# Kernel optimization log

Measured on AMD Instinct MI355X. Metric: run time of the kernel, lower is better.

Reference implementation:

```python
import jax, jax.numpy as jnp
import numpy as np

N_NODES = 50000
N_EDGES = 800000
IN_FEATS = 128
HIDDEN = 128
DNN_H = 256
N_CLASSES = 40


def setup_inputs() -> dict:
    key = jax.random.key(0)
    ks = jax.random.split(key, 12)
    features = jax.random.normal(ks[0], (N_NODES, IN_FEATS), dtype=jnp.float32)
    src = jax.random.randint(ks[1], (N_EDGES,), 0, N_NODES, dtype=jnp.int32)
    dst = jax.random.randint(ks[2], (N_EDGES,), 0, N_NODES, dtype=jnp.int32)
    def lin(k, fi, fo):
        s = 1.0 / np.sqrt(fi)
        return jax.random.uniform(k, (fi, fo), jnp.float32, -s, s)
    W1 = lin(ks[3], IN_FEATS, HIDDEN)
    b1 = jnp.zeros((HIDDEN,), jnp.float32)
    W2 = lin(ks[4], HIDDEN, HIDDEN)
    b2 = jnp.zeros((HIDDEN,), jnp.float32)
    Wd1 = lin(ks[5], HIDDEN, DNN_H)
    bd1 = jnp.zeros((DNN_H,), jnp.float32)
    Wd2 = lin(ks[6], DNN_H, N_CLASSES)
    bd2 = jnp.zeros((N_CLASSES,), jnp.float32)
    return {"features": features, "src": src, "dst": dst,
            "W1": W1, "b1": b1, "W2": W2, "b2": b2,
            "Wd1": Wd1, "bd1": bd1, "Wd2": Wd2, "bd2": bd2}


def _graph_conv(x, src, dst, W, b):
    # dgl GraphConv, norm='both': D_out^{-1/2} -> sum-aggregate -> D_in^{-1/2} -> linear -> relu
    ones = jnp.ones((src.shape[0],), x.dtype)
    deg_out = jax.ops.segment_sum(ones, src, num_segments=N_NODES)
    deg_in = jax.ops.segment_sum(ones, dst, num_segments=N_NODES)
    inv_sqrt_out = jax.lax.rsqrt(jnp.maximum(deg_out, 1.0))  # clamp zero-degree to 1 like dgl
    inv_sqrt_in = jax.lax.rsqrt(jnp.maximum(deg_in, 1.0))
    x = x * inv_sqrt_out[:, None]
    h = jax.ops.segment_sum(x[src], dst, num_segments=N_NODES)  # [N, d] sparse SpMM
    h = h * inv_sqrt_in[:, None]
    return jax.nn.relu(h @ W + b)


def reference(features, src, dst, W1, b1, W2, b2, Wd1, bd1, Wd2, bd2):
    h = _graph_conv(features, src, dst, W1, b1)   # dropout = identity (eval)
    h = _graph_conv(h, src, dst, W2, b2)
    # DNN: Linear -> LeakyReLU(0.01) -> (dropout identity), x2
    h = jax.nn.leaky_relu(h @ Wd1 + bd1, negative_slope=0.01)
    h = jax.nn.leaky_relu(h @ Wd2 + bd2, negative_slope=0.01)
    return h
```

## Files before the change

kernel.cpp:

```cpp
#include <hip/hip_runtime.h>


#define SCAN_B 256

typedef __attribute__((ext_vector_type(8))) short short8v;
typedef __attribute__((ext_vector_type(4))) float f32x4;

__global__ void k_scanA(const int* __restrict__ deg_in, int* __restrict__ incl,
                        int* __restrict__ bsum, int N) {
    __shared__ int s[SCAN_B];
    int t = threadIdx.x, i = blockIdx.x * SCAN_B + t;
    int v = (i < N) ? deg_in[i] : 0;
    s[t] = v; __syncthreads();
    for (int o = 1; o < SCAN_B; o <<= 1) {
        int x = (t >= o) ? s[t - o] : 0;
        __syncthreads();
        s[t] += x;
        __syncthreads();
    }
    if (i < N) incl[i] = s[t];
    if (t == SCAN_B - 1) bsum[blockIdx.x] = s[t];
}

__global__ void k_scanB(int* __restrict__ bsum, int NB) {
    __shared__ int s[SCAN_B];
    int t = threadIdx.x;
    int v = (t < NB) ? bsum[t] : 0;
    s[t] = v; __syncthreads();
    for (int o = 1; o < SCAN_B; o <<= 1) {
        int x = (t >= o) ? s[t - o] : 0;
        __syncthreads();
        s[t] += x;
        __syncthreads();
    }
    if (t < NB) bsum[t] = s[t] - v;
}

__global__ void k_scanC(const int* __restrict__ deg_in, const int* __restrict__ deg_out,
                        int* __restrict__ row_ptr, const int* __restrict__ bsum,
                        float* __restrict__ inv_in, float* __restrict__ inv_out,
                        int N, int E) {
    int t = threadIdx.x, i = blockIdx.x * SCAN_B + t;
    if (i < N) {
        int di = deg_in[i];
        row_ptr[i] = row_ptr[i] - di + bsum[blockIdx.x];
        inv_in[i]  = rsqrtf(fmaxf((float)di, 1.0f));
        inv_out[i] = rsqrtf(fmaxf((float)deg_out[i], 1.0f));
    }
    if (i == 0) row_ptr[N] = E;
}

__global__ void k_scatter3(const int* __restrict__ src, const int* __restrict__ dst,
                           const int* __restrict__ row_ptr, const int* __restrict__ rank,
                           const float* __restrict__ inv_out,
                           int2* __restrict__ edges, int E) {
    int i = blockIdx.x * blockDim.x + threadIdx.x;
    if (i < E) {
        int s = src[i];
        int2 p;
        p.x = s;
        p.y = __float_as_int(inv_out[s]);
        edges[row_ptr[dst[i]] + rank[i]] = p;
    }
}

__global__ void k_gather2(const float* __restrict__ X, const int2* __restrict__ edges,
                          const int* __restrict__ row_ptr, const float* __restrict__ inv_in,
                          const float* __restrict__ bias, float* __restrict__ Y, int N) {
    int lane = threadIdx.x & 31;
    int row = blockIdx.x * 8 + (threadIdx.x >> 5);
    if (row >= N) return;
    int rs = row_ptr[row], re = row_ptr[row + 1];
    float4 acc = {0.f, 0.f, 0.f, 0.f};
    int e = rs;
    #define LDROW(s) (*reinterpret_cast<const float4*>(&X[(size_t)(s) * 128 + lane * 4]))
    for (; e + 8 <= re; e += 8) {
        int2 p0 = edges[e],     p1 = edges[e + 1], p2 = edges[e + 2], p3 = edges[e + 3];
        int2 p4 = edges[e + 4], p5 = edges[e + 5], p6 = edges[e + 6], p7 = edges[e + 7];
        float4 x0 = LDROW(p0.x), x1 = LDROW(p1.x), x2 = LDROW(p2.x), x3 = LDROW(p3.x);
        float4 x4 = LDROW(p4.x), x5 = LDROW(p5.x), x6 = LDROW(p6.x), x7 = LDROW(p7.x);
        float c0 = __int_as_float(p0.y), c1 = __int_as_float(p1.y);
        float c2 = __int_as_float(p2.y), c3 = __int_as_float(p3.y);
        float c4 = __int_as_float(p4.y), c5 = __int_as_float(p5.y);
        float c6 = __int_as_float(p6.y), c7 = __int_as_float(p7.y);
        acc.x += c0*x0.x + c1*x1.x + c2*x2.x + c3*x3.x + c4*x4.x + c5*x5.x + c6*x6.x + c7*x7.x;
        acc.y += c0*x0.y + c1*x1.y + c2*x2.y + c3*x3.y + c4*x4.y + c5*x5.y + c6*x6.y + c7*x7.y;
        acc.z += c0*x0.z + c1*x1.z + c2*x2.z + c3*x3.z + c4*x4.z + c5*x5.z + c6*x6.z + c7*x7.z;
        acc.w += c0*x0.w + c1*x1.w + c2*x2.w + c3*x3.w + c4*x4.w + c5*x5.w + c6*x6.w + c7*x7.w;
    }
    for (; e + 4 <= re; e += 4) {
        int2 p0 = edges[e], p1 = edges[e + 1], p2 = edges[e + 2], p3 = edges[e + 3];
        float4 x0 = LDROW(p0.x), x1 = LDROW(p1.x), x2 = LDROW(p2.x), x3 = LDROW(p3.x);
        float c0 = __int_as_float(p0.y), c1 = __int_as_float(p1.y);
        float c2 = __int_as_float(p2.y), c3 = __int_as_float(p3.y);
        acc.x += c0*x0.x + c1*x1.x + c2*x2.x + c3*x3.x;
        acc.y += c0*x0.y + c1*x1.y + c2*x2.y + c3*x3.y;
        acc.z += c0*x0.z + c1*x1.z + c2*x2.z + c3*x3.z;
        acc.w += c0*x0.w + c1*x1.w + c2*x2.w + c3*x3.w;
    }
    for (; e < re; ++e) {
        int2 p = edges[e];
        float c = __int_as_float(p.y);
        float4 xv = LDROW(p.x);
        acc.x += c * xv.x; acc.y += c * xv.y; acc.z += c * xv.z; acc.w += c * xv.w;
    }
    #undef LDROW
    float si = inv_in[row];
    float4 b4 = *reinterpret_cast<const float4*>(&bias[lane * 4]);
    float4 o;
    o.x = fmaxf(fmaf(acc.x, si, b4.x), 0.f);
    o.y = fmaxf(fmaf(acc.y, si, b4.y), 0.f);
    o.z = fmaxf(fmaf(acc.z, si, b4.z), 0.f);
    o.w = fmaxf(fmaf(acc.w, si, b4.w), 0.f);
    *reinterpret_cast<float4*>(&Y[(size_t)row * 128 + lane * 4]) = o;
}

__device__ inline unsigned short bf16_rne(float f) {
    unsigned int u = __float_as_uint(f);
    u += 0x7fffu + ((u >> 16) & 1u);
    return (unsigned short)(u >> 16);
}

__device__ inline void split1(float a, unsigned short& h, unsigned short& l) {
    unsigned short hh = bf16_rne(a);
    float hf = __uint_as_float((unsigned int)hh << 16);
    l = bf16_rne(a - hf);
    h = hh;
}

template<int K, int N, int ACT, bool DEG>
__global__ __launch_bounds__(256) void k_gemm_mfma(const float* __restrict__ A,
                                                   const float* __restrict__ W,
                                                   const float* __restrict__ bias,
                                                   float* __restrict__ C, int M,
                                                   const int* __restrict__ src,
                                                   const int* __restrict__ dst,
                                                   int* __restrict__ deg_out,
                                                   int* __restrict__ deg_in,
                                                   int* __restrict__ rank, int E, int epb,
                                                   int gmm, int degb) {
    __shared__ unsigned short Bh[64 * K], Bl[64 * K];
    __shared__ unsigned short Ah[128 * 32], Al[128 * 32];

    int t = threadIdx.x;
    int m0, cb;
    if (DEG) {
        int bid = blockIdx.x;
        if (bid < degb) {
            int base = bid * epb;
            int end = min(E, base + epb);
            for (int i = base + t; i < end; i += 256) {
                atomicAdd(&deg_out[src[i]], 1);
                rank[i] = atomicAdd(&deg_in[dst[i]], 1);
            }
            return;
        }
        int tile = bid - degb;
        m0 = (tile % gmm) * 128;
        cb = (tile / gmm) * 64;
    } else {
        m0 = blockIdx.x * 128;
        cb = blockIdx.y * 64;
    }

    {
        int c = t & 63;
        int kb = (t >> 6) * (K / 4);
        bool cok = (N % 64 == 0) || (cb + c < N);
        for (int j = 0; j < K / 4; ++j) {
            int k = kb + j;
            float v = cok ? W[(size_t)k * N + cb + c] : 0.f;
            unsigned short hi, lo; split1(v, hi, lo);
            int byte = (c * 2 * K + 2 * k) ^ ((c & 7) << 4);
            Bh[byte >> 1] = hi;
            Bl[byte >> 1] = lo;
        }
    }

    f32x4 acc[4][2];
    #pragma unroll
    for (int i = 0; i < 4; ++i)
        #pragma unroll
        for (int j = 0; j < 2; ++j)
            acc[i][j] = (f32x4){0.f, 0.f, 0.f, 0.f};

    int lane = t & 63;
    int wave = t >> 6;
    int wm = wave >> 1, wn = wave & 1;
    int lr = lane & 15, lg = lane >> 4;

    for (int kt = 0; kt < K / 32; ++kt) {
        __syncthreads();
        #pragma unroll
        for (int i = 0; i < 4; ++i) {
            int g = i * 256 + t;
            int r = g >> 3;
            int kq = (g & 7) * 4;
            int gr = m0 + r;
            float4 v = {0.f, 0.f, 0.f, 0.f};
            if (gr < M) v = *reinterpret_cast<const float4*>(&A[(size_t)gr * K + kt * 32 + kq]);
            ushort4 h4, l4;
            split1(v.x, h4.x, l4.x);
            split1(v.y, h4.y, l4.y);
            split1(v.z, h4.z, l4.z);
            split1(v.w, h4.w, l4.w);
            int byte = (r * 64 + 2 * kq) ^ ((r & 7) << 4);
            *reinterpret_cast<ushort4*>(&Ah[byte >> 1]) = h4;
            *reinterpret_cast<ushort4*>(&Al[byte >> 1]) = l4;
        }
        __syncthreads();

        short8v bhf[2], blf[2];
        #pragma unroll
        for (int nf = 0; nf < 2; ++nf) {
            int c = wn * 32 + nf * 16 + lr;
            int byte = (c * 2 * K + 2 * (kt * 32 + lg * 8)) ^ ((c & 7) << 4);
            bhf[nf] = *reinterpret_cast<const short8v*>(&Bh[byte >> 1]);
            blf[nf] = *reinterpret_cast<const short8v*>(&Bl[byte >> 1]);
        }
        #pragma unroll
        for (int mf = 0; mf < 4; ++mf) {
            int r = wm * 64 + mf * 16 + lr;
            int byte = (r * 64 + 2 * (lg * 8)) ^ ((r & 7) << 4);
            short8v ahf = *reinterpret_cast<const short8v*>(&Ah[byte >> 1]);
            short8v alf = *reinterpret_cast<const short8v*>(&Al[byte >> 1]);
            #pragma unroll
            for (int nf = 0; nf < 2; ++nf) {
                acc[mf][nf] = __builtin_amdgcn_mfma_f32_16x16x32_bf16(ahf, bhf[nf], acc[mf][nf], 0, 0, 0);
                acc[mf][nf] = __builtin_amdgcn_mfma_f32_16x16x32_bf16(ahf, blf[nf], acc[mf][nf], 0, 0, 0);
                acc[mf][nf] = __builtin_amdgcn_mfma_f32_16x16x32_bf16(alf, bhf[nf], acc[mf][nf], 0, 0, 0);
            }
        }
    }

    #pragma unroll
    for (int mf = 0; mf < 4; ++mf) {
        #pragma unroll
        for (int nf = 0; nf < 2; ++nf) {
            int col = cb + wn * 32 + nf * 16 + lr;
            if ((N % 64 != 0) && col >= N) continue;
            float bv = (ACT < 2) ? bias[col] : 0.f;
            #pragma unroll
            for (int rg = 0; rg < 4; ++rg) {
                int row = m0 + wm * 64 + mf * 16 + lg * 4 + rg;
                if (row < M) {
                    float v = acc[mf][nf][rg];
                    if (ACT == 0) v = fmaxf(v + bv, 0.f);
                    else if (ACT == 1) { v += bv; v = (v > 0.f) ? v : 0.01f * v; }
                    C[(size_t)row * N + col] = v;
                }
            }
        }
    }
}

extern "C" void kernel_launch(void* const* d_in, const int* in_sizes, int n_in,
                              void* d_out, int out_size, void* d_ws, size_t ws_size,
                              hipStream_t stream) {
    const float* feat = (const float*)d_in[0];
    const int*   src  = (const int*)d_in[1];
    const int*   dst  = (const int*)d_in[2];
    const float* W1   = (const float*)d_in[3];
    const float* b1   = (const float*)d_in[4];
    const float* W2   = (const float*)d_in[5];
    const float* b2   = (const float*)d_in[6];
    const float* Wd1  = (const float*)d_in[7];
    const float* bd1  = (const float*)d_in[8];
    const float* Wd2  = (const float*)d_in[9];
    const float* bd2  = (const float*)d_in[10];
    float* out = (float*)d_out;

    const int N = in_sizes[0] / 128;
    const int E = in_sizes[1];

    char* ws = (char*)d_ws;
    size_t off = 0;
    auto alloc = [&](size_t bytes) -> void* {
        void* p = ws + off;
        off += (bytes + 255) & ~(size_t)255;
        return p;
    };
    int* deg_out  = (int*)alloc((size_t)N * 4);
    int* deg_in   = (int*)alloc((size_t)N * 4);
    int* row_ptr  = (int*)alloc((size_t)(N + 1) * 4);
    int* bsum     = (int*)alloc(SCAN_B * 4);
    int* rank     = (int*)alloc((size_t)E * 4);
    int2* edges   = (int2*)alloc((size_t)E * 8);
    float* inv_out = (float*)alloc((size_t)N * 4);
    float* inv_in  = (float*)alloc((size_t)N * 4);
    float* bufA = (float*)alloc((size_t)N * 128 * 4);
    float* bufB = (float*)alloc((size_t)N * 128 * 4);
    float* hd   = (float*)alloc((size_t)N * 256 * 4);

    size_t zspan = (char*)deg_in + (size_t)N * 4 - (char*)deg_out;
    hipMemsetAsync(deg_out, 0, zspan, stream);

    int gE = (E + 255) / 256;
    int gN = (N + SCAN_B - 1) / SCAN_B;
    int gG = (N + 7) / 8;
    int gMM = (N + 127) / 128;

    const int DEGB = 512;
    int epb = (E + DEGB - 1) / DEGB;
    k_gemm_mfma<128, 128, 2, true><<<DEGB + gMM * 2, 256, 0, stream>>>(
        feat, W1, nullptr, bufA, N, src, dst, deg_out, deg_in, rank, E, epb, gMM, DEGB);

    k_scanA<<<gN, SCAN_B, 0, stream>>>(deg_in, row_ptr, bsum, N);
    k_scanB<<<1, SCAN_B, 0, stream>>>(bsum, gN);
    k_scanC<<<gN, SCAN_B, 0, stream>>>(deg_in, deg_out, row_ptr, bsum, inv_in, inv_out, N, E);
    k_scatter3<<<gE, 256, 0, stream>>>(src, dst, row_ptr, rank, inv_out, edges, E);

    k_gather2<<<gG, 256, 0, stream>>>(bufA, edges, row_ptr, inv_in, b1, bufB, N);
    k_gemm_mfma<128, 128, 2, false><<<dim3(gMM, 2), 256, 0, stream>>>(
        bufB, W2, nullptr, bufA, N, nullptr, nullptr, nullptr, nullptr, nullptr, 0, 0, 0, 0);
    k_gather2<<<gG, 256, 0, stream>>>(bufA, edges, row_ptr, inv_in, b2, bufB, N);
    k_gemm_mfma<128, 256, 1, false><<<dim3(gMM, 4), 256, 0, stream>>>(
        bufB, Wd1, bd1, hd, N, nullptr, nullptr, nullptr, nullptr, nullptr, 0, 0, 0, 0);
    k_gemm_mfma<256, 40, 1, false><<<dim3(gMM, 1), 256, 0, stream>>>(
        hd, Wd2, bd2, out, N, nullptr, nullptr, nullptr, nullptr, nullptr, 0, 0, 0, 0);
}
```

Baseline: 337.3 us.

## Fuse SpMM gather with following dense GEMM into one gconv kernel

Replaces each gather-then-GEMM pair with a single kernel. It aggregates 64 rows of neighbour features, applies bias and ReLU, splits the result to bf16 hi/lo in shared memory, and multiplies by the next weight matrix with MFMA. This drops the intermediate round trip of the N×128 activation through global memory and one launch per layer. In exchange the gather phase runs with fewer blocks (64 rows per block) and each block reloads the weights, which may cut latency hiding during the irregular gather. The degree-counting loop is also unrolled by four so more loads and atomics are in flight.

Result: slower. 470.2 us (+39.4%).

```diff
diff --git a/kernel.cpp b/kernel.cpp
--- a/kernel.cpp
+++ b/kernel.cpp
@@ -64,57 +64,6 @@
     }
 }
 
-__global__ void k_gather2(const float* __restrict__ X, const int2* __restrict__ edges,
-                          const int* __restrict__ row_ptr, const float* __restrict__ inv_in,
-                          const float* __restrict__ bias, float* __restrict__ Y, int N) {
-    int lane = threadIdx.x & 31;
-    int row = blockIdx.x * 8 + (threadIdx.x >> 5);
-    if (row >= N) return;
-    int rs = row_ptr[row], re = row_ptr[row + 1];
-    float4 acc = {0.f, 0.f, 0.f, 0.f};
-    int e = rs;
-    #define LDROW(s) (*reinterpret_cast<const float4*>(&X[(size_t)(s) * 128 + lane * 4]))
-    for (; e + 8 <= re; e += 8) {
-        int2 p0 = edges[e],     p1 = edges[e + 1], p2 = edges[e + 2], p3 = edges[e + 3];
-        int2 p4 = edges[e + 4], p5 = edges[e + 5], p6 = edges[e + 6], p7 = edges[e + 7];
-        float4 x0 = LDROW(p0.x), x1 = LDROW(p1.x), x2 = LDROW(p2.x), x3 = LDROW(p3.x);
-        float4 x4 = LDROW(p4.x), x5 = LDROW(p5.x), x6 = LDROW(p6.x), x7 = LDROW(p7.x);
-        float c0 = __int_as_float(p0.y), c1 = __int_as_float(p1.y);
-        float c2 = __int_as_float(p2.y), c3 = __int_as_float(p3.y);
-        float c4 = __int_as_float(p4.y), c5 = __int_as_float(p5.y);
-        float c6 = __int_as_float(p6.y), c7 = __int_as_float(p7.y);
-        acc.x += c0*x0.x + c1*x1.x + c2*x2.x + c3*x3.x + c4*x4.x + c5*x5.x + c6*x6.x + c7*x7.x;
-        acc.y += c0*x0.y + c1*x1.y + c2*x2.y + c3*x3.y + c4*x4.y + c5*x5.y + c6*x6.y + c7*x7.y;
-        acc.z += c0*x0.z + c1*x1.z + c2*x2.z + c3*x3.z + c4*x4.z + c5*x5.z + c6*x6.z + c7*x7.z;
-        acc.w += c0*x0.w + c1*x1.w + c2*x2.w + c3*x3.w + c4*x4.w + c5*x5.w + c6*x6.w + c7*x7.w;
-    }
-    for (; e + 4 <= re; e += 4) {
-        int2 p0 = edges[e], p1 = edges[e + 1], p2 = edges[e + 2], p3 = edges[e + 3];
-        float4 x0 = LDROW(p0.x), x1 = LDROW(p1.x), x2 = LDROW(p2.x), x3 = LDROW(p3.x);
-        float c0 = __int_as_float(p0.y), c1 = __int_as_float(p1.y);
-        float c2 = __int_as_float(p2.y), c3 = __int_as_float(p3.y);
-        acc.x += c0*x0.x + c1*x1.x + c2*x2.x + c3*x3.x;
-        acc.y += c0*x0.y + c1*x1.y + c2*x2.y + c3*x3.y;
-        acc.z += c0*x0.z + c1*x1.z + c2*x2.z + c3*x3.z;
-        acc.w += c0*x0.w + c1*x1.w + c2*x2.w + c3*x3.w;
-    }
-    for (; e < re; ++e) {
-        int2 p = edges[e];
-        float c = __int_as_float(p.y);
-        float4 xv = LDROW(p.x);
-        acc.x += c * xv.x; acc.y += c * xv.y; acc.z += c * xv.z; acc.w += c * xv.w;
-    }
-    #undef LDROW
-    float si = inv_in[row];
-    float4 b4 = *reinterpret_cast<const float4*>(&bias[lane * 4]);
-    float4 o;
-    o.x = fmaxf(fmaf(acc.x, si, b4.x), 0.f);
-    o.y = fmaxf(fmaf(acc.y, si, b4.y), 0.f);
-    o.z = fmaxf(fmaf(acc.z, si, b4.z), 0.f);
-    o.w = fmaxf(fmaf(acc.w, si, b4.w), 0.f);
-    *reinterpret_cast<float4*>(&Y[(size_t)row * 128 + lane * 4]) = o;
-}
-
 __device__ inline unsigned short bf16_rne(float f) {
     unsigned int u = __float_as_uint(f);
     u += 0x7fffu + ((u >> 16) & 1u);
@@ -126,6 +75,136 @@
     float hf = __uint_as_float((unsigned int)hh << 16);
     l = bf16_rne(a - hf);
     h = hh;
+}
+
+template<int NOUT, int ACTPOST>
+__global__ __launch_bounds__(256) void k_gconv(const float* __restrict__ X,
+                                               const int2* __restrict__ edges,
+                                               const int* __restrict__ row_ptr,
+                                               const float* __restrict__ inv_in,
+                                               const float* __restrict__ bias_pre,
+                                               const float* __restrict__ W,
+                                               const float* __restrict__ bias_post,
+                                               float* __restrict__ C, int M) {
+    __shared__ unsigned short Ah[64 * 128], Al[64 * 128];
+    __shared__ unsigned short Bh[32 * NOUT], Bl[32 * NOUT];
+
+    int t = threadIdx.x;
+    int rows0 = blockIdx.x * 64;
+    int grp = t >> 5, lane = t & 31;
+
+    for (int r8 = 0; r8 < 8; ++r8) {
+        int rloc = grp * 8 + r8;
+        int row = rows0 + rloc;
+        float4 acc = {0.f, 0.f, 0.f, 0.f};
+        if (row < M) {
+            int rs = row_ptr[row], re = row_ptr[row + 1];
+            int e = rs;
+            #define LDROW(s) (*reinterpret_cast<const float4*>(&X[(size_t)(s) * 128 + lane * 4]))
+            for (; e + 8 <= re; e += 8) {
+                int2 p0 = edges[e],     p1 = edges[e + 1], p2 = edges[e + 2], p3 = edges[e + 3];
+                int2 p4 = edges[e + 4], p5 = edges[e + 5], p6 = edges[e + 6], p7 = edges[e + 7];
+                float4 x0 = LDROW(p0.x), x1 = LDROW(p1.x), x2 = LDROW(p2.x), x3 = LDROW(p3.x);
+                float4 x4 = LDROW(p4.x), x5 = LDROW(p5.x), x6 = LDROW(p6.x), x7 = LDROW(p7.x);
+                float c0 = __int_as_float(p0.y), c1 = __int_as_float(p1.y);
+                float c2 = __int_as_float(p2.y), c3 = __int_as_float(p3.y);
+                float c4 = __int_as_float(p4.y), c5 = __int_as_float(p5.y);
+                float c6 = __int_as_float(p6.y), c7 = __int_as_float(p7.y);
+                acc.x += c0*x0.x + c1*x1.x + c2*x2.x + c3*x3.x + c4*x4.x + c5*x5.x + c6*x6.x + c7*x7.x;
+                acc.y += c0*x0.y + c1*x1.y + c2*x2.y + c3*x3.y + c4*x4.y + c5*x5.y + c6*x6.y + c7*x7.y;
+                acc.z += c0*x0.z + c1*x1.z + c2*x2.z + c3*x3.z + c4*x4.z + c5*x5.z + c6*x6.z + c7*x7.z;
+                acc.w += c0*x0.w + c1*x1.w + c2*x2.w + c3*x3.w + c4*x4.w + c5*x5.w + c6*x6.w + c7*x7.w;
+            }
+            for (; e < re; ++e) {
+                int2 p = edges[e];
+                float c = __int_as_float(p.y);
+                float4 xv = LDROW(p.x);
+                acc.x += c * xv.x; acc.y += c * xv.y; acc.z += c * xv.z; acc.w += c * xv.w;
+            }
+            #undef LDROW
+            float si = inv_in[row];
+            float4 b4 = *reinterpret_cast<const float4*>(&bias_pre[lane * 4]);
+            acc.x = fmaxf(fmaf(acc.x, si, b4.x), 0.f);
+            acc.y = fmaxf(fmaf(acc.y, si, b4.y), 0.f);
+            acc.z = fmaxf(fmaf(acc.z, si, b4.z), 0.f);
+            acc.w = fmaxf(fmaf(acc.w, si, b4.w), 0.f);
+        }
+        ushort4 h4, l4;
+        split1(acc.x, h4.x, l4.x);
+        split1(acc.y, h4.y, l4.y);
+        split1(acc.z, h4.z, l4.z);
+        split1(acc.w, h4.w, l4.w);
+        int byte = (rloc * 256 + lane * 8) ^ ((rloc & 7) << 4);
+        *reinterpret_cast<ushort4*>(&Ah[byte >> 1]) = h4;
+        *reinterpret_cast<ushort4*>(&Al[byte >> 1]) = l4;
+    }
+    __syncthreads();
+
+    int wave = t >> 6;
+    int wm = wave >> 1, wn = wave & 1;
+    int lr = t & 15, lg = (t & 63) >> 4;
+
+    f32x4 acc2[2][NOUT / 32];
+    #pragma unroll
+    for (int i = 0; i < 2; ++i)
+        #pragma unroll
+        for (int j = 0; j < NOUT / 32; ++j)
+            acc2[i][j] = (f32x4){0.f, 0.f, 0.f, 0.f};
+
+    for (int kt = 0; kt < 4; ++kt) {
+        #pragma unroll
+        for (int j = 0; j < 32 * NOUT / 256; ++j) {
+            int idx = j * 256 + t;
+            int kloc = idx / NOUT, c = idx % NOUT;
+            float v = W[(size_t)(kt * 32 + kloc) * NOUT + c];
+            unsigned short hi, lo; split1(v, hi, lo);
+            int byte = (c * 64 + 2 * kloc) ^ ((c & 7) << 4);
+            Bh[byte >> 1] = hi;
+            Bl[byte >> 1] = lo;
+        }
+        __syncthreads();
+
+        short8v bhf[NOUT / 32], blf[NOUT / 32];
+        #pragma unroll
+        for (int nf = 0; nf < NOUT / 32; ++nf) {
+            int cloc = wn * (NOUT / 2) + nf * 16 + lr;
+            int byte = (cloc * 64 + 2 * (lg * 8)) ^ ((cloc & 7) << 4);
+            bhf[nf] = *reinterpret_cast<const short8v*>(&Bh[byte >> 1]);
+            blf[nf] = *reinterpret_cast<const short8v*>(&Bl[byte >> 1]);
+        }
+        #pragma unroll
+        for (int mf = 0; mf < 2; ++mf) {
+            int rloc = wm * 32 + mf * 16 + lr;
+            int byte = (rloc * 256 + 2 * (kt * 32 + lg * 8)) ^ ((rloc & 7) << 4);
+            short8v ahf = *reinterpret_cast<const short8v*>(&Ah[byte >> 1]);
+            short8v alf = *reinterpret_cast<const short8v*>(&Al[byte >> 1]);
+            #pragma unroll
+            for (int nf = 0; nf < NOUT / 32; ++nf) {
+                acc2[mf][nf] = __builtin_amdgcn_mfma_f32_16x16x32_bf16(ahf, bhf[nf], acc2[mf][nf], 0, 0, 0);
+                acc2[mf][nf] = __builtin_amdgcn_mfma_f32_16x16x32_bf16(ahf, blf[nf], acc2[mf][nf], 0, 0, 0);
+                acc2[mf][nf] = __builtin_amdgcn_mfma_f32_16x16x32_bf16(alf, bhf[nf], acc2[mf][nf], 0, 0, 0);
+            }
+        }
+        __syncthreads();
+    }
+
+    #pragma unroll
+    for (int mf = 0; mf < 2; ++mf) {
+        #pragma unroll
+        for (int nf = 0; nf < NOUT / 32; ++nf) {
+            int col = wn * (NOUT / 2) + nf * 16 + lr;
+            float bv = (ACTPOST == 1) ? bias_post[col] : 0.f;
+            #pragma unroll
+            for (int rg = 0; rg < 4; ++rg) {
+                int row = rows0 + wm * 32 + mf * 16 + lg * 4 + rg;
+                if (row < M) {
+                    float v = acc2[mf][nf][rg];
+                    if (ACTPOST == 1) { v += bv; v = (v > 0.f) ? v : 0.01f * v; }
+                    C[(size_t)row * NOUT + col] = v;
+                }
+            }
+        }
+    }
 }
 
 template<int K, int N, int ACT, bool DEG>
@@ -149,7 +228,21 @@
         if (bid < degb) {
             int base = bid * epb;
             int end = min(E, base + epb);
-            for (int i = base + t; i < end; i += 256) {
+            int i = base + t;
+            for (; i + 768 < end; i += 1024) {
+                int sA = src[i], sB = src[i + 256], sC = src[i + 512], sD = src[i + 768];
+                int dA = dst[i], dB = dst[i + 256], dC = dst[i + 512], dD = dst[i + 768];
+                atomicAdd(&deg_out[sA], 1);
+                atomicAdd(&deg_out[sB], 1);
+                atomicAdd(&deg_out[sC], 1);
+                atomicAdd(&deg_out[sD], 1);
+                int rA = atomicAdd(&deg_in[dA], 1);
+                int rB = atomicAdd(&deg_in[dB], 1);
+                int rC = atomicAdd(&deg_in[dC], 1);
+                int rD = atomicAdd(&deg_in[dD], 1);
+                rank[i] = rA; rank[i + 256] = rB; rank[i + 512] = rC; rank[i + 768] = rD;
+            }
+            for (; i < end; i += 256) {
                 atomicAdd(&deg_out[src[i]], 1);
                 rank[i] = atomicAdd(&deg_in[dst[i]], 1);
             }
@@ -297,8 +390,8 @@
 
     int gE = (E + 255) / 256;
     int gN = (N + SCAN_B - 1) / SCAN_B;
-    int gG = (N + 7) / 8;
     int gMM = (N + 127) / 128;
+    int gGC = (N + 63) / 64;
 
     const int DEGB = 512;
     int epb = (E + DEGB - 1) / DEGB;
@@ -310,12 +403,10 @@
     k_scanC<<<gN, SCAN_B, 0, stream>>>(deg_in, deg_out, row_ptr, bsum, inv_in, inv_out, N, E);
     k_scatter3<<<gE, 256, 0, stream>>>(src, dst, row_ptr, rank, inv_out, edges, E);
 
-    k_gather2<<<gG, 256, 0, stream>>>(bufA, edges, row_ptr, inv_in, b1, bufB, N);
-    k_gemm_mfma<128, 128, 2, false><<<dim3(gMM, 2), 256, 0, stream>>>(
-        bufB, W2, nullptr, bufA, N, nullptr, nullptr, nullptr, nullptr, nullptr, 0, 0, 0, 0);
-    k_gather2<<<gG, 256, 0, stream>>>(bufA, edges, row_ptr, inv_in, b2, bufB, N);
-    k_gemm_mfma<128, 256, 1, false><<<dim3(gMM, 4), 256, 0, stream>>>(
-        bufB, Wd1, bd1, hd, N, nullptr, nullptr, nullptr, nullptr, nullptr, 0, 0, 0, 0);
+    k_gconv<128, 2><<<gGC, 256, 0, stream>>>(bufA, edges, row_ptr, inv_in, b1, W2,
+                                             nullptr, bufB, N);
+    k_gconv<256, 1><<<gGC, 256, 0, stream>>>(bufB, edges, row_ptr, inv_in, b2, Wd1,
+                                             bd1, hd, N);
     k_gemm_mfma<256, 40, 1, false><<<dim3(gMM, 1), 256, 0, stream>>>(
         hd, Wd2, bd2, out, N, nullptr, nullptr, nullptr, nullptr, nullptr, 0, 0, 0, 0);
 }
```
